# Optimization experiments

Measured on AMD Instinct MI355X. Metric: run time of the kernel, lower is better.

Reference implementation:

```python
import jax, jax.numpy as jnp
import numpy as np

K = 3          # kernel_size
P = K // 2     # padding


def setup_inputs() -> dict:
    key = jax.random.key(0)
    # [B, C, H, W]; first C-4 channels are per-class probabilities, last 4 are box offsets
    points = jax.random.normal(key, (4, 84, 512, 512), dtype=jnp.float32)
    return {"points": points}


def reference(points):
    # Peak (point) NMS: keep a pixel iff torch.argmax over its KxK window of
    # max-class-probability lands exactly on the window center.
    # torch.argmax returns the FIRST flat index attaining the max, so the center
    # survives iff it is strictly greater than every earlier (row-major) window
    # element and >= every later element.
    probs = jnp.max(points[:, :-4], axis=1)            # [B, H, W]
    B, H, W = probs.shape
    padded = jnp.pad(probs, ((0, 0), (P, P), (P, P)))  # zero pad, matches F.pad default
    center_idx = P * K + P
    mask = jnp.ones((B, H, W), dtype=bool)
    for di in range(K):                                # small fixed K*K loop (8 iters)
        for dj in range(K):
            idx = di * K + dj
            if idx == center_idx:
                continue
            nb = padded[:, di:di + H, dj:dj + W]       # neighbor value at this offset
            cmp = (probs > nb) if idx < center_idx else (probs >= nb)
            mask = mask & cmp
    # non-peaks zeroed across ALL channels, exactly like the zeros_like + scatter
    return points * mask[:, None, :, :].astype(points.dtype)
```

## Files before the change

### kernel.cpp

```cpp
#include <hip/hip_runtime.h>

#define BB 4
#define CC 84
#define CM 80
#define HH 512
#define WW 512
#define HWSZ (HH * WW)
#define PG (HWSZ / 4)

template <int NCH>
__global__ __launch_bounds__(256) void partial_max_kernel(const float* __restrict__ pts,
                                                          float* __restrict__ partial) {
    constexpr int CPC = CM / NCH;
    int tid = blockIdx.x * blockDim.x + threadIdx.x;
    int pg  = tid & (PG - 1);
    int r   = tid >> 16;
    int chunk = (NCH == 1) ? 0 : (r % NCH);
    int b     = (NCH == 1) ? r : (r / NCH);

    const float4* base = (const float4*)pts + ((size_t)b * CC + chunk * CPC) * PG + pg;
    float4 m = base[0];
#pragma unroll 8
    for (int c = 1; c < CPC; ++c) {
        float4 v = base[(size_t)c * PG];
        m.x = fmaxf(m.x, v.x);
        m.y = fmaxf(m.y, v.y);
        m.z = fmaxf(m.z, v.z);
        m.w = fmaxf(m.w, v.w);
    }
    ((float4*)partial)[((size_t)chunk * BB + b) * PG + pg] = m;
}

template <int NCH>
__global__ __launch_bounds__(256) void combine_kernel(float* __restrict__ partial) {
    int tid = blockIdx.x * blockDim.x + threadIdx.x;
    int pg  = tid & (PG - 1);
    int b   = tid >> 16;
    float4* p = (float4*)partial;
    float4 m = p[(size_t)b * PG + pg];
#pragma unroll
    for (int ch = 1; ch < NCH; ++ch) {
        float4 v = p[((size_t)ch * BB + b) * PG + pg];
        m.x = fmaxf(m.x, v.x);
        m.y = fmaxf(m.y, v.y);
        m.z = fmaxf(m.z, v.z);
        m.w = fmaxf(m.w, v.w);
    }
    p[(size_t)b * PG + pg] = m;
}

__global__ __launch_bounds__(256) void mask_kernel(const float* __restrict__ probs,
                                                   float* __restrict__ mask) {
    int tid = blockIdx.x * blockDim.x + threadIdx.x;
    int pg  = tid & (PG - 1);
    int b   = tid >> 16;
    int off = pg << 2;
    int h   = off >> 9;
    int w0  = off & (WW - 1);

    const float* pb = probs + (size_t)b * HWSZ;

    float rows[3][6];
#pragma unroll
    for (int r = 0; r < 3; ++r) {
        int hh = h + r - 1;
        bool hv = (hh >= 0) & (hh < HH);
        const float* rp = pb + hh * WW;
#pragma unroll
        for (int ci = 0; ci < 6; ++ci) {
            int ww = w0 + ci - 1;
            bool wv = (ww >= 0) & (ww < WW);
            rows[r][ci] = (hv & wv) ? rp[ww] : 0.0f;
        }
    }

    float4 fm;
    float* fmp = &fm.x;
#pragma unroll
    for (int j = 0; j < 4; ++j) {
        float v = rows[1][j + 1];
        bool m = (v >  rows[0][j]) & (v >  rows[0][j + 1]) & (v >  rows[0][j + 2])
               & (v >  rows[1][j]) & (v >= rows[1][j + 2])
               & (v >= rows[2][j]) & (v >= rows[2][j + 1]) & (v >= rows[2][j + 2]);
        fmp[j] = m ? 1.0f : 0.0f;
    }
    ((float4*)mask)[(size_t)b * PG + pg] = fm;
}

__global__ __launch_bounds__(256) void mul_kernel(const float* __restrict__ pts,
                                                  const float* __restrict__ mask,
                                                  float* __restrict__ out) {
    int tid = blockIdx.x * blockDim.x + threadIdx.x;
    int pg  = tid & (PG - 1);
    int r   = tid >> 16;
    int c   = r % CC;
    int b   = r / CC;

    float4 m = ((const float4*)mask)[(size_t)b * PG + pg];
    size_t idx = ((size_t)b * CC + c) * PG + pg;

    int nz = (__float_as_uint(m.x) | __float_as_uint(m.y) |
              __float_as_uint(m.z) | __float_as_uint(m.w));
    if (nz) {
        float4 v = ((const float4*)pts)[idx];
        float4 o;
        o.x = v.x * m.x;
        o.y = v.y * m.y;
        o.z = v.z * m.z;
        o.w = v.w * m.w;
        ((float4*)out)[idx] = o;
    } else {
        ((float4*)out)[idx] = make_float4(0.f, 0.f, 0.f, 0.f);
    }
}

__global__ __launch_bounds__(256) void probs_kernel_fb(const float* __restrict__ pts,
                                                       float* __restrict__ probs) {
    int tid = blockIdx.x * blockDim.x + threadIdx.x;
    int pix = tid << 2;
    int b   = pix >> 18;
    int off = pix & (HWSZ - 1);
    const float4* base = (const float4*)(pts + (size_t)b * CC * HWSZ + off);
    float4 m = base[0];
#pragma unroll 4
    for (int c = 1; c < CM; ++c) {
        float4 v = base[c * (HWSZ / 4)];
        m.x = fmaxf(m.x, v.x); m.y = fmaxf(m.y, v.y);
        m.z = fmaxf(m.z, v.z); m.w = fmaxf(m.w, v.w);
    }
    ((float4*)probs)[tid] = m;
}

__global__ __launch_bounds__(256) void nms_mul_kernel_fb(const float* __restrict__ pts,
                                                         const float* __restrict__ probs,
                                                         float* __restrict__ out) {
    int tid = blockIdx.x * blockDim.x + threadIdx.x;
    int pix = tid << 2;
    int b   = pix >> 18;
    int off = pix & (HWSZ - 1);
    int h   = off >> 9;
    int w0  = off & (WW - 1);
    const float* pb = probs + b * HWSZ;
    float rows[3][6];
#pragma unroll
    for (int r = 0; r < 3; ++r) {
        int hh = h + r - 1;
        bool hv = (hh >= 0) & (hh < HH);
        const float* rp = pb + hh * WW;
#pragma unroll
        for (int ci = 0; ci < 6; ++ci) {
            int ww = w0 + ci - 1;
            bool wv = (ww >= 0) & (ww < WW);
            rows[r][ci] = (hv & wv) ? rp[ww] : 0.0f;
        }
    }
    float fm[4];
    bool any = false;
#pragma unroll
    for (int j = 0; j < 4; ++j) {
        float v = rows[1][j + 1];
        bool m = (v >  rows[0][j]) & (v >  rows[0][j + 1]) & (v >  rows[0][j + 2])
               & (v >  rows[1][j]) & (v >= rows[1][j + 2])
               & (v >= rows[2][j]) & (v >= rows[2][j + 1]) & (v >= rows[2][j + 2]);
        fm[j] = m ? 1.0f : 0.0f;
        any |= m;
    }
    size_t bo = (size_t)b * CC * HWSZ + off;
    const float4* src = (const float4*)(pts + bo);
    float4* dst = (float4*)(out + bo);
    if (any) {
#pragma unroll 4
        for (int c = 0; c < CC; ++c) {
            float4 v = src[c * (HWSZ / 4)];
            float4 o;
            o.x = v.x * fm[0]; o.y = v.y * fm[1];
            o.z = v.z * fm[2]; o.w = v.w * fm[3];
            dst[c * (HWSZ / 4)] = o;
        }
    } else {
        float4 z = make_float4(0.f, 0.f, 0.f, 0.f);
#pragma unroll 4
        for (int c = 0; c < CC; ++c) dst[c * (HWSZ / 4)] = z;
    }
}

extern "C" void kernel_launch(void* const* d_in, const int* in_sizes, int n_in,
                              void* d_out, int out_size, void* d_ws, size_t ws_size,
                              hipStream_t stream) {
    const float* pts = (const float*)d_in[0];
    float* out = (float*)d_out;
    float* ws  = (float*)d_ws;

    const size_t MB4 = (size_t)BB * HWSZ * sizeof(float);
    dim3 blk(256);
    int npg_threads = BB * PG;
    dim3 grd_pg(npg_threads / 256);

    if (ws_size >= 5 * MB4) {
        constexpr int NCH = 4;
        float* partial = ws;
        float* probs   = ws;
        float* mask    = ws + NCH * (size_t)BB * HWSZ;
        partial_max_kernel<NCH><<<dim3(BB * NCH * PG / 256), blk, 0, stream>>>(pts, partial);
        combine_kernel<NCH><<<grd_pg, blk, 0, stream>>>(partial);
        mask_kernel<<<grd_pg, blk, 0, stream>>>(probs, mask);
        mul_kernel<<<dim3(BB * CC * PG / 256), blk, 0, stream>>>(pts, mask, out);
    } else if (ws_size >= 3 * MB4) {
        constexpr int NCH = 2;
        float* partial = ws;
        float* probs   = ws;
        float* mask    = ws + NCH * (size_t)BB * HWSZ;
        partial_max_kernel<NCH><<<dim3(BB * NCH * PG / 256), blk, 0, stream>>>(pts, partial);
        combine_kernel<NCH><<<grd_pg, blk, 0, stream>>>(partial);
        mask_kernel<<<grd_pg, blk, 0, stream>>>(probs, mask);
        mul_kernel<<<dim3(BB * CC * PG / 256), blk, 0, stream>>>(pts, mask, out);
    } else if (ws_size >= 2 * MB4) {
        float* probs = ws;
        float* mask  = ws + (size_t)BB * HWSZ;
        partial_max_kernel<1><<<grd_pg, blk, 0, stream>>>(pts, probs);
        mask_kernel<<<grd_pg, blk, 0, stream>>>(probs, mask);
        mul_kernel<<<dim3(BB * CC * PG / 256), blk, 0, stream>>>(pts, mask, out);
    } else {
        float* probs = ws;
        probs_kernel_fb<<<grd_pg, blk, 0, stream>>>(pts, probs);
        nms_mul_kernel_fb<<<grd_pg, blk, 0, stream>>>(pts, probs, out);
    }
}
```

Before: 624.4 us.

## Fuse partial-max combine into mask kernel, add nontemporal loads, reorder mul grid

Removes the separate combine kernel by having the mask kernel take the max over the four channel-chunk partials directly for each stencil neighbor. Input loads and output stores use nontemporal hints to avoid polluting cache with streamed data. The mul kernel grid is remapped so consecutive blocks share the same spatial tile across channels, improving mask reuse in cache. The stencil now does four partial loads per neighbor (redundant reads), and the NCH=2 and NCH=1 workspace paths are dropped.

Result: no change. 613.8 us (-1.7%).

```diff
diff --git a/kernel.cpp b/kernel.cpp
--- a/kernel.cpp
+++ b/kernel.cpp
@@ -7,50 +7,40 @@
 #define WW 512
 #define HWSZ (HH * WW)
 #define PG (HWSZ / 4)
-
-template <int NCH>
+#define NCH 4
+#define CPC (CM / NCH)
+
+typedef float v4f __attribute__((ext_vector_type(4)));
+
+static __device__ __forceinline__ v4f vmax4(v4f a, v4f b) {
+    v4f r;
+    r.x = fmaxf(a.x, b.x);
+    r.y = fmaxf(a.y, b.y);
+    r.z = fmaxf(a.z, b.z);
+    r.w = fmaxf(a.w, b.w);
+    return r;
+}
+
 __global__ __launch_bounds__(256) void partial_max_kernel(const float* __restrict__ pts,
                                                           float* __restrict__ partial) {
-    constexpr int CPC = CM / NCH;
     int tid = blockIdx.x * blockDim.x + threadIdx.x;
     int pg  = tid & (PG - 1);
     int r   = tid >> 16;
-    int chunk = (NCH == 1) ? 0 : (r % NCH);
-    int b     = (NCH == 1) ? r : (r / NCH);
-
-    const float4* base = (const float4*)pts + ((size_t)b * CC + chunk * CPC) * PG + pg;
-    float4 m = base[0];
-#pragma unroll 8
+    int chunk = r % NCH;
+    int b     = r / NCH;
+
+    const v4f* base = (const v4f*)pts + ((size_t)b * CC + chunk * CPC) * PG + pg;
+    v4f m = __builtin_nontemporal_load(base);
+#pragma unroll 5
     for (int c = 1; c < CPC; ++c) {
-        float4 v = base[(size_t)c * PG];
-        m.x = fmaxf(m.x, v.x);
-        m.y = fmaxf(m.y, v.y);
-        m.z = fmaxf(m.z, v.z);
-        m.w = fmaxf(m.w, v.w);
-    }
-    ((float4*)partial)[((size_t)chunk * BB + b) * PG + pg] = m;
-}
-
-template <int NCH>
-__global__ __launch_bounds__(256) void combine_kernel(float* __restrict__ partial) {
-    int tid = blockIdx.x * blockDim.x + threadIdx.x;
-    int pg  = tid & (PG - 1);
-    int b   = tid >> 16;
-    float4* p = (float4*)partial;
-    float4 m = p[(size_t)b * PG + pg];
-#pragma unroll
-    for (int ch = 1; ch < NCH; ++ch) {
-        float4 v = p[((size_t)ch * BB + b) * PG + pg];
-        m.x = fmaxf(m.x, v.x);
-        m.y = fmaxf(m.y, v.y);
-        m.z = fmaxf(m.z, v.z);
-        m.w = fmaxf(m.w, v.w);
-    }
-    p[(size_t)b * PG + pg] = m;
-}
-
-__global__ __launch_bounds__(256) void mask_kernel(const float* __restrict__ probs,
-                                                   float* __restrict__ mask) {
+        v4f v = __builtin_nontemporal_load(base + (size_t)c * PG);
+        m = vmax4(m, v);
+    }
+    ((v4f*)partial)[((size_t)chunk * BB + b) * PG + pg] = m;
+}
+
+__global__ __launch_bounds__(256) void fused_mask_kernel(const float* __restrict__ partial,
+                                                         float* __restrict__ mask) {
     int tid = blockIdx.x * blockDim.x + threadIdx.x;
     int pg  = tid & (PG - 1);
     int b   = tid >> 16;
@@ -58,60 +48,68 @@
     int h   = off >> 9;
     int w0  = off & (WW - 1);
 
-    const float* pb = probs + (size_t)b * HWSZ;
-
     float rows[3][6];
 #pragma unroll
     for (int r = 0; r < 3; ++r) {
         int hh = h + r - 1;
         bool hv = (hh >= 0) & (hh < HH);
-        const float* rp = pb + hh * WW;
 #pragma unroll
         for (int ci = 0; ci < 6; ++ci) {
             int ww = w0 + ci - 1;
             bool wv = (ww >= 0) & (ww < WW);
-            rows[r][ci] = (hv & wv) ? rp[ww] : 0.0f;
+            float v = 0.0f;
+            if (hv & wv) {
+                int pidx = hh * WW + ww;
+                v = partial[(size_t)(0 * BB + b) * HWSZ + pidx];
+#pragma unroll
+                for (int ch = 1; ch < NCH; ++ch)
+                    v = fmaxf(v, partial[(size_t)(ch * BB + b) * HWSZ + pidx]);
+            }
+            rows[r][ci] = v;
         }
     }
 
-    float4 fm;
-    float* fmp = &fm.x;
+    v4f fm;
 #pragma unroll
     for (int j = 0; j < 4; ++j) {
         float v = rows[1][j + 1];
         bool m = (v >  rows[0][j]) & (v >  rows[0][j + 1]) & (v >  rows[0][j + 2])
                & (v >  rows[1][j]) & (v >= rows[1][j + 2])
                & (v >= rows[2][j]) & (v >= rows[2][j + 1]) & (v >= rows[2][j + 2]);
-        fmp[j] = m ? 1.0f : 0.0f;
-    }
-    ((float4*)mask)[(size_t)b * PG + pg] = fm;
+        float f = m ? 1.0f : 0.0f;
+        if (j == 0) fm.x = f;
+        else if (j == 1) fm.y = f;
+        else if (j == 2) fm.z = f;
+        else fm.w = f;
+    }
+    ((v4f*)mask)[(size_t)b * PG + pg] = fm;
 }
 
 __global__ __launch_bounds__(256) void mul_kernel(const float* __restrict__ pts,
                                                   const float* __restrict__ mask,
                                                   float* __restrict__ out) {
-    int tid = blockIdx.x * blockDim.x + threadIdx.x;
-    int pg  = tid & (PG - 1);
-    int r   = tid >> 16;
-    int c   = r % CC;
-    int b   = r / CC;
-
-    float4 m = ((const float4*)mask)[(size_t)b * PG + pg];
+    int gid = blockIdx.x;
+    int c   = gid % CC;
+    int pc  = gid / CC;
+    int b   = pc >> 8;
+    int pg  = ((pc & 255) << 8) + threadIdx.x;
+
+    v4f m = ((const v4f*)mask)[(size_t)b * PG + pg];
     size_t idx = ((size_t)b * CC + c) * PG + pg;
 
-    int nz = (__float_as_uint(m.x) | __float_as_uint(m.y) |
-              __float_as_uint(m.z) | __float_as_uint(m.w));
+    unsigned nz = (__float_as_uint(m.x) | __float_as_uint(m.y) |
+                   __float_as_uint(m.z) | __float_as_uint(m.w));
+    v4f o;
     if (nz) {
-        float4 v = ((const float4*)pts)[idx];
-        float4 o;
+        v4f v = __builtin_nontemporal_load((const v4f*)pts + idx);
         o.x = v.x * m.x;
         o.y = v.y * m.y;
         o.z = v.z * m.z;
         o.w = v.w * m.w;
-        ((float4*)out)[idx] = o;
     } else {
-        ((float4*)out)[idx] = make_float4(0.f, 0.f, 0.f, 0.f);
-    }
+        o.x = 0.f; o.y = 0.f; o.z = 0.f; o.w = 0.f;
+    }
+    __builtin_nontemporal_store(o, (v4f*)out + idx);
 }
 
 __global__ __launch_bounds__(256) void probs_kernel_fb(const float* __restrict__ pts,
@@ -193,33 +191,14 @@
 
     const size_t MB4 = (size_t)BB * HWSZ * sizeof(float);
     dim3 blk(256);
-    int npg_threads = BB * PG;
-    dim3 grd_pg(npg_threads / 256);
-
-    if (ws_size >= 5 * MB4) {
-        constexpr int NCH = 4;
+    dim3 grd_pg(BB * PG / 256);
+
+    if (ws_size >= (NCH + 1) * MB4) {
         float* partial = ws;
-        float* probs   = ws;
-        float* mask    = ws + NCH * (size_t)BB * HWSZ;
-        partial_max_kernel<NCH><<<dim3(BB * NCH * PG / 256), blk, 0, stream>>>(pts, partial);
-        combine_kernel<NCH><<<grd_pg, blk, 0, stream>>>(partial);
-        mask_kernel<<<grd_pg, blk, 0, stream>>>(probs, mask);
-        mul_kernel<<<dim3(BB * CC * PG / 256), blk, 0, stream>>>(pts, mask, out);
-    } else if (ws_size >= 3 * MB4) {
-        constexpr int NCH = 2;
-        float* partial = ws;
-        float* probs   = ws;
-        float* mask    = ws + NCH * (size_t)BB * HWSZ;
-        partial_max_kernel<NCH><<<dim3(BB * NCH * PG / 256), blk, 0, stream>>>(pts, partial);
-        combine_kernel<NCH><<<grd_pg, blk, 0, stream>>>(partial);
-        mask_kernel<<<grd_pg, blk, 0, stream>>>(probs, mask);
-        mul_kernel<<<dim3(BB * CC * PG / 256), blk, 0, stream>>>(pts, mask, out);
-    } else if (ws_size >= 2 * MB4) {
-        float* probs = ws;
-        float* mask  = ws + (size_t)BB * HWSZ;
-        partial_max_kernel<1><<<grd_pg, blk, 0, stream>>>(pts, probs);
-        mask_kernel<<<grd_pg, blk, 0, stream>>>(probs, mask);
-        mul_kernel<<<dim3(BB * CC * PG / 256), blk, 0, stream>>>(pts, mask, out);
+        float* mask    = ws + (size_t)NCH * BB * HWSZ;
+        partial_max_kernel<<<dim3(BB * NCH * PG / 256), blk, 0, stream>>>(pts, partial);
+        fused_mask_kernel<<<grd_pg, blk, 0, stream>>>(partial, mask);
+        mul_kernel<<<dim3(BB * CC * (PG / 256)), blk, 0, stream>>>(pts, mask, out);
     } else {
         float* probs = ws;
         probs_kernel_fb<<<grd_pg, blk, 0, stream>>>(pts, probs);
```
